# Optimization experiments

Hardware: AMD Instinct MI355X
Metric: run time of the kernel (lower is better)

## Reference

```python
import jax, jax.numpy as jnp
import numpy as np

B, LM, LX, D = 16, 1024, 1024, 768


def setup_inputs() -> dict:
    key = jax.random.key(0)
    k1, k2, k3, k4 = jax.random.split(key, 4)
    main = jax.random.normal(k1, (B, LM, D), dtype=jnp.float32)
    x = jax.random.normal(k2, (B, LX, D), dtype=jnp.float32)
    # keras 'uniform' init ~ U(-0.05, 0.05); scale to keep activations sane
    W = jax.random.uniform(k3, (D, D), dtype=jnp.float32, minval=-0.05, maxval=0.05)
    w = jax.random.uniform(k4, (2 * D, 1), dtype=jnp.float32, minval=-0.05, maxval=0.05)
    return {"main": main, "x": x, "W": W, "w": w}


def reference(main, x, W, w):
    # bilinear co-attention scores: (main @ W) . x^T -> (B, LM, LX)
    proj = jnp.einsum('bmd,de->bme', main, W)            # (B, LM, D)
    scores = jnp.einsum('bme,bne->bmn', proj, x)         # (B, LM, LX) -- no softmax in original
    A = jnp.einsum('bmn,bnd->bmd', scores, x)            # attended features (B, LM, D)
    s = main - A
    m = main * A
    outputs = jnp.concatenate([s, m], axis=-1)           # (B, LM, 2D)
    beta = jnp.einsum('bmk,k->bm', outputs, w[:, 0])     # (B, LM) -- raw, no softmax
    pooled = jnp.einsum('bm,bmk->bk', beta, outputs)     # weighted-sum pooling (B, 2D)
    return pooled
```

## Files before the change

kernel.cpp:

```cpp
#include <hip/hip_runtime.h>

constexpr int kB  = 16;
constexpr int kLM = 1024;
constexpr int kLX = 1024;
constexpr int kD  = 768;

using short8 = __attribute__((ext_vector_type(8))) short;
using f32x4  = __attribute__((ext_vector_type(4))) float;

__device__ __forceinline__ unsigned short f2bf(float f) {
    unsigned u = __float_as_uint(f);
    u = (u + 0x7FFF + ((u >> 16) & 1)) >> 16;
    return (unsigned short)u;
}
__device__ __forceinline__ float bf2f(unsigned short h) {
    return __uint_as_float(((unsigned)h) << 16);
}

__device__ __forceinline__ void gl_lds16(const unsigned short* g, unsigned short* l) {
    auto gp = (const __attribute__((address_space(1))) unsigned int*)g;
    auto lp = (__attribute__((address_space(3))) unsigned int*)l;
    __builtin_amdgcn_global_load_lds(gp, lp, 16, 0, 0);
}

__global__ __launch_bounds__(256) void transpose_cvt_kernel(
    const float* __restrict__ x, unsigned short* __restrict__ xT) {
    __shared__ float tile[64][65];
    const int b  = blockIdx.z;
    const int l0 = blockIdx.x * 64;
    const int d0 = blockIdx.y * 64;
    const int t  = threadIdx.x;
    const int tx = t & 15, ty = t >> 4;
    const float* xb = x + ((size_t)b * kLX + l0) * kD + d0;
#pragma unroll
    for (int p = 0; p < 4; ++p) {
        int r = p * 16 + ty;
        float4 v = *(const float4*)(xb + (size_t)r * kD + tx * 4);
        *(float4*)&tile[r][tx * 4] = v;
    }
    __syncthreads();
    unsigned short* xTb = xT + ((size_t)b * kD + d0) * kLX + l0;
#pragma unroll
    for (int p = 0; p < 4; ++p) {
        int dr = p * 16 + ty;
        ushort4 o;
        o.x = f2bf(tile[tx * 4 + 0][dr]);
        o.y = f2bf(tile[tx * 4 + 1][dr]);
        o.z = f2bf(tile[tx * 4 + 2][dr]);
        o.w = f2bf(tile[tx * 4 + 3][dr]);
        *(ushort4*)(xTb + (size_t)dr * kLX + tx * 4) = o;
    }
}

__global__ __launch_bounds__(256) void cvt_bf16_dual_kernel(
    const float* __restrict__ a, unsigned short* __restrict__ oa, int n4a,
    const float* __restrict__ b, unsigned short* __restrict__ ob, int n4b) {
    int i = blockIdx.x * blockDim.x + threadIdx.x;
    const float* src; unsigned short* dst; int idx;
    if (i < n4a) { src = a; dst = oa; idx = i; }
    else { idx = i - n4a; if (idx >= n4b) return; src = b; dst = ob; }
    float4 v = ((const float4*)src)[idx];
    ushort4 o;
    o.x = f2bf(v.x); o.y = f2bf(v.y); o.z = f2bf(v.z); o.w = f2bf(v.w);
    ((ushort4*)dst)[idx] = o;
}

__global__ __launch_bounds__(256) void gemm_nt_bf16_kernel(
    const unsigned short* __restrict__ A, const unsigned short* __restrict__ B,
    unsigned short* __restrict__ C, int M, int N, int K,
    long sA, long sB, long sC) {
    __shared__ unsigned short Asm[2][128 * 32];
    __shared__ unsigned short Bsm[2][128 * 32];
    const int b  = blockIdx.z;
    const int i0 = blockIdx.x * 128;
    const int j0 = blockIdx.y * 128;
    const int t    = threadIdx.x;
    const int wave = t >> 6, lane = t & 63;
    const int wr = (wave >> 1) * 64, wc = (wave & 1) * 64;
    const int quad = lane >> 4, l15 = lane & 15;

    const unsigned short* Ab = A + (size_t)b * sA + (size_t)i0 * K;
    const unsigned short* Bb = B + (size_t)b * sB + (size_t)j0 * K;

    const int c0 = wave * 64 + lane;
    const int c1 = 256 + wave * 64 + lane;
    auto chunk_off = [&](int c) -> size_t {
        int sr = c >> 3, s = c & 7;
        int tt = s ^ (sr & 7);
        int r  = sr * 2 + (tt >> 2);
        int q  = tt & 3;
        return (size_t)r * K + q * 8;
    };
    const size_t off0 = chunk_off(c0);
    const size_t off1 = chunk_off(c1);

    const int sfr = ((l15 & 1) * 4 + quad) ^ ((l15 >> 1) & 7);
    const int aOff = (wr >> 1) * 64 + (l15 >> 1) * 64 + sfr * 8;
    const int bOff = (wc >> 1) * 64 + (l15 >> 1) * 64 + sfr * 8;

    f32x4 acc[4][4];
    const f32x4 z = {0.f, 0.f, 0.f, 0.f};
#pragma unroll
    for (int i = 0; i < 4; ++i)
#pragma unroll
        for (int j = 0; j < 4; ++j) acc[i][j] = z;

    const int T = K >> 5;
    gl_lds16(Ab + off0, Asm[0] + c0 * 8);
    gl_lds16(Ab + off1, Asm[0] + c1 * 8);
    gl_lds16(Bb + off0, Bsm[0] + c0 * 8);
    gl_lds16(Bb + off1, Bsm[0] + c1 * 8);

    int buf = 0;
    for (int kt = 0; kt < T; ++kt) {
        __syncthreads();
        if (kt + 1 < T) {
            const size_t k = (size_t)(kt + 1) << 5;
            unsigned short* An = Asm[buf ^ 1];
            unsigned short* Bn = Bsm[buf ^ 1];
            gl_lds16(Ab + off0 + k, An + c0 * 8);
            gl_lds16(Ab + off1 + k, An + c1 * 8);
            gl_lds16(Bb + off0 + k, Bn + c0 * 8);
            gl_lds16(Bb + off1 + k, Bn + c1 * 8);
        }
        const unsigned short* aP = Asm[buf] + aOff;
        const unsigned short* bP = Bsm[buf] + bOff;
        short8 af[4], bg[4];
#pragma unroll
        for (int i = 0; i < 4; ++i) af[i] = *(const short8*)(aP + i * 512);
#pragma unroll
        for (int j = 0; j < 4; ++j) bg[j] = *(const short8*)(bP + j * 512);
#pragma unroll
        for (int i = 0; i < 4; ++i)
#pragma unroll
            for (int j = 0; j < 4; ++j)
                acc[i][j] = __builtin_amdgcn_mfma_f32_16x16x32_bf16(
                    af[i], bg[j], acc[i][j], 0, 0, 0);
        buf ^= 1;
    }

    unsigned short* Cb = C + (size_t)b * sC + (size_t)(i0 + wr) * N + j0 + wc;
#pragma unroll
    for (int i = 0; i < 4; ++i)
#pragma unroll
        for (int j = 0; j < 4; ++j)
#pragma unroll
            for (int r = 0; r < 4; ++r)
                Cb[(size_t)(i * 16 + quad * 4 + r) * N + j * 16 + l15] =
                    f2bf(acc[i][j][r]);
}

__global__ __launch_bounds__(256) void pool_kernel(
    const float* __restrict__ mainp, const unsigned short* __restrict__ Aout,
    const float* __restrict__ w, float* __restrict__ out) {
    const int b     = blockIdx.y;
    const int chunk = blockIdx.x;
    const int wave  = threadIdx.x >> 6, lane = threadIdx.x & 63;
    float w1[12], w2[12], ps[12], pm[12];
#pragma unroll
    for (int s = 0; s < 12; ++s) {
        w1[s] = w[s * 64 + lane];
        w2[s] = w[kD + s * 64 + lane];
        ps[s] = 0.f; pm[s] = 0.f;
    }
#pragma unroll
    for (int rr = 0; rr < 4; ++rr) {
        const int row = chunk * 16 + rr * 4 + wave;
        const float* mr = mainp + ((size_t)b * kLM + row) * kD;
        const unsigned short* ar = Aout + ((size_t)b * kLM + row) * kD;
        float sv[12], mv[12], acc = 0.f;
#pragma unroll
        for (int s = 0; s < 12; ++s) {
            float m_ = mr[s * 64 + lane];
            float a_ = bf2f(ar[s * 64 + lane]);
            sv[s] = m_ - a_;
            mv[s] = m_ * a_;
            acc += sv[s] * w1[s] + mv[s] * w2[s];
        }
#pragma unroll
        for (int off = 32; off; off >>= 1) acc += __shfl_xor(acc, off);
#pragma unroll
        for (int s = 0; s < 12; ++s) { ps[s] += acc * sv[s]; pm[s] += acc * mv[s]; }
    }
    float* ob = out + (size_t)b * 2 * kD;
#pragma unroll
    for (int s = 0; s < 12; ++s) {
        atomicAdd(&ob[s * 64 + lane], ps[s]);
        atomicAdd(&ob[kD + s * 64 + lane], pm[s]);
    }
}

extern "C" void kernel_launch(void* const* d_in, const int* in_sizes, int n_in,
                              void* d_out, int out_size, void* d_ws, size_t ws_size,
                              hipStream_t stream) {
    const float* mainp = (const float*)d_in[0];
    const float* x     = (const float*)d_in[1];
    const float* W     = (const float*)d_in[2];
    const float* w     = (const float*)d_in[3];
    float* out = (float*)d_out;

    char* p = (char*)d_ws;
    unsigned short* xT    = (unsigned short*)p; p += (size_t)kB * kD * kLX * 2;
    unsigned short* mainb = (unsigned short*)p; p += (size_t)kB * kLM * kD * 2;
    unsigned short* Wb    = (unsigned short*)p; p += (size_t)kD * kD * 2;
    unsigned short* G     = (unsigned short*)p; p += (size_t)kB * kD * kD * 2;
    unsigned short* Mt    = (unsigned short*)p; p += (size_t)kB * kD * kD * 2;
    unsigned short* Ao    = (unsigned short*)p; p += (size_t)kB * kLM * kD * 2;

    hipMemsetAsync(out, 0, (size_t)kB * 2 * kD * sizeof(float), stream);

    transpose_cvt_kernel<<<dim3(kLX / 64, kD / 64, kB), 256, 0, stream>>>(x, xT);
    {
        int n4a = kB * kLM * kD / 4;
        int n4b = kD * kD / 4;
        cvt_bf16_dual_kernel<<<(n4a + n4b + 255) / 256, 256, 0, stream>>>(
            mainp, mainb, n4a, W, Wb, n4b);
    }
    gemm_nt_bf16_kernel<<<dim3(kD / 128, kD / 128, kB), 256, 0, stream>>>(
        xT, xT, G, kD, kD, kLX, (long)kD * kLX, (long)kD * kLX, (long)kD * kD);
    gemm_nt_bf16_kernel<<<dim3(kD / 128, kD / 128, kB), 256, 0, stream>>>(
        G, Wb, Mt, kD, kD, kD, (long)kD * kD, 0L, (long)kD * kD);
    gemm_nt_bf16_kernel<<<dim3(kLM / 128, kD / 128, kB), 256, 0, stream>>>(
        mainb, Mt, Ao, kLM, kD, kD, (long)kLM * kD, (long)kD * kD, (long)kLM * kD);
    pool_kernel<<<dim3(kLM / 16, kB), 256, 0, stream>>>(mainp, Ao, w, out);
}
```

Measured before the change: 264.8 us.

## Fuse fp32-to-bf16 conversion into GEMM loaders and shrink N tile to 64

Removes the standalone conversion kernel for main and W. The GEMM now loads fp32 operands through registers, converts them to bf16 and writes them into swizzled LDS, with a two-stage register prefetch. The GEMM tile also shrinks from 128x128 to 128x64, with each wave owning 32x64, and launch bounds request 4 blocks per CU. This saves a full pass over main and doubles block count for better CU coverage. In exchange the fp32 loads go through registers instead of direct-to-LDS, main is re-read at fp32 width across N tiles, and per-tile data reuse is lower.

```diff
diff --git a/kernel.cpp b/kernel.cpp
--- a/kernel.cpp
+++ b/kernel.cpp
@@ -21,6 +21,21 @@
     auto gp = (const __attribute__((address_space(1))) unsigned int*)g;
     auto lp = (__attribute__((address_space(3))) unsigned int*)l;
     __builtin_amdgcn_global_load_lds(gp, lp, 16, 0, 0);
+}
+
+__device__ __forceinline__ void writeChunk(unsigned short* dst, float4 lo, float4 hi) {
+    union { short8 v; unsigned short u[8]; } o;
+    o.u[0] = f2bf(lo.x); o.u[1] = f2bf(lo.y); o.u[2] = f2bf(lo.z); o.u[3] = f2bf(lo.w);
+    o.u[4] = f2bf(hi.x); o.u[5] = f2bf(hi.y); o.u[6] = f2bf(hi.z); o.u[7] = f2bf(hi.w);
+    *(short8*)dst = o.v;
+}
+
+__device__ __forceinline__ size_t chunk_off(int c, int K) {
+    int sr = c >> 3, s = c & 7;
+    int tt = s ^ (sr & 7);
+    int r  = sr * 2 + (tt >> 2);
+    int q  = tt & 3;
+    return (size_t)r * K + q * 8;
 }
 
 __global__ __launch_bounds__(256) void transpose_cvt_kernel(
@@ -52,86 +67,117 @@
     }
 }
 
-__global__ __launch_bounds__(256) void cvt_bf16_dual_kernel(
-    const float* __restrict__ a, unsigned short* __restrict__ oa, int n4a,
-    const float* __restrict__ b, unsigned short* __restrict__ ob, int n4b) {
-    int i = blockIdx.x * blockDim.x + threadIdx.x;
-    const float* src; unsigned short* dst; int idx;
-    if (i < n4a) { src = a; dst = oa; idx = i; }
-    else { idx = i - n4a; if (idx >= n4b) return; src = b; dst = ob; }
-    float4 v = ((const float4*)src)[idx];
-    ushort4 o;
-    o.x = f2bf(v.x); o.y = f2bf(v.y); o.z = f2bf(v.z); o.w = f2bf(v.w);
-    ((ushort4*)dst)[idx] = o;
-}
-
-__global__ __launch_bounds__(256) void gemm_nt_bf16_kernel(
-    const unsigned short* __restrict__ A, const unsigned short* __restrict__ B,
+template <bool AFP32, bool BFP32>
+__global__ __launch_bounds__(256, 4) void gemm_nt_kernel(
+    const void* __restrict__ Av, const void* __restrict__ Bv,
     unsigned short* __restrict__ C, int M, int N, int K,
     long sA, long sB, long sC) {
     __shared__ unsigned short Asm[2][128 * 32];
-    __shared__ unsigned short Bsm[2][128 * 32];
+    __shared__ unsigned short Bsm[2][64 * 32];
     const int b  = blockIdx.z;
     const int i0 = blockIdx.x * 128;
-    const int j0 = blockIdx.y * 128;
+    const int j0 = blockIdx.y * 64;
     const int t    = threadIdx.x;
     const int wave = t >> 6, lane = t & 63;
-    const int wr = (wave >> 1) * 64, wc = (wave & 1) * 64;
     const int quad = lane >> 4, l15 = lane & 15;
 
-    const unsigned short* Ab = A + (size_t)b * sA + (size_t)i0 * K;
-    const unsigned short* Bb = B + (size_t)b * sB + (size_t)j0 * K;
-
-    const int c0 = wave * 64 + lane;
-    const int c1 = 256 + wave * 64 + lane;
-    auto chunk_off = [&](int c) -> size_t {
-        int sr = c >> 3, s = c & 7;
-        int tt = s ^ (sr & 7);
-        int r  = sr * 2 + (tt >> 2);
-        int q  = tt & 3;
-        return (size_t)r * K + q * 8;
-    };
-    const size_t off0 = chunk_off(c0);
-    const size_t off1 = chunk_off(c1);
-
-    const int sfr = ((l15 & 1) * 4 + quad) ^ ((l15 >> 1) & 7);
-    const int aOff = (wr >> 1) * 64 + (l15 >> 1) * 64 + sfr * 8;
-    const int bOff = (wc >> 1) * 64 + (l15 >> 1) * 64 + sfr * 8;
-
-    f32x4 acc[4][4];
+    const unsigned short* Abh = AFP32 ? nullptr
+        : (const unsigned short*)Av + (size_t)b * sA + (size_t)i0 * K;
+    const unsigned short* Bbh = BFP32 ? nullptr
+        : (const unsigned short*)Bv + (size_t)b * sB + (size_t)j0 * K;
+    const float* Abf = AFP32
+        ? (const float*)Av + (size_t)b * sA + (size_t)i0 * K : nullptr;
+    const float* Bbf = BFP32
+        ? (const float*)Bv + (size_t)b * sB + (size_t)j0 * K : nullptr;
+
+    const int cA0 = t, cA1 = t + 256, cB = t;
+    const size_t offA0 = chunk_off(cA0, K);
+    const size_t offA1 = chunk_off(cA1, K);
+    const size_t offB  = chunk_off(cB, K);
+
+    const int sfr  = ((l15 & 1) * 4 + quad) ^ ((l15 >> 1) & 7);
+    const int aOff = wave * 1024 + (l15 >> 1) * 64 + sfr * 8;
+    const int bOff = (l15 >> 1) * 64 + sfr * 8;
+
+    f32x4 acc[2][4];
     const f32x4 z = {0.f, 0.f, 0.f, 0.f};
 #pragma unroll
-    for (int i = 0; i < 4; ++i)
+    for (int i = 0; i < 2; ++i)
 #pragma unroll
         for (int j = 0; j < 4; ++j) acc[i][j] = z;
 
     const int T = K >> 5;
-    gl_lds16(Ab + off0, Asm[0] + c0 * 8);
-    gl_lds16(Ab + off1, Asm[0] + c1 * 8);
-    gl_lds16(Bb + off0, Bsm[0] + c0 * 8);
-    gl_lds16(Bb + off1, Bsm[0] + c1 * 8);
+    float4 pa0, pa1, pa2, pa3, pb0, pb1;
+
+    if constexpr (AFP32) {
+        float4 a0 = *(const float4*)(Abf + offA0);
+        float4 a1 = *(const float4*)(Abf + offA0 + 4);
+        float4 a2 = *(const float4*)(Abf + offA1);
+        float4 a3 = *(const float4*)(Abf + offA1 + 4);
+        writeChunk(Asm[0] + cA0 * 8, a0, a1);
+        writeChunk(Asm[0] + cA1 * 8, a2, a3);
+    } else {
+        gl_lds16(Abh + offA0, Asm[0] + cA0 * 8);
+        gl_lds16(Abh + offA1, Asm[0] + cA1 * 8);
+    }
+    if constexpr (BFP32) {
+        float4 b0 = *(const float4*)(Bbf + offB);
+        float4 b1 = *(const float4*)(Bbf + offB + 4);
+        writeChunk(Bsm[0] + cB * 8, b0, b1);
+    } else {
+        gl_lds16(Bbh + offB, Bsm[0] + cB * 8);
+    }
+    if constexpr (AFP32) {
+        pa0 = *(const float4*)(Abf + offA0 + 32);
+        pa1 = *(const float4*)(Abf + offA0 + 36);
+        pa2 = *(const float4*)(Abf + offA1 + 32);
+        pa3 = *(const float4*)(Abf + offA1 + 36);
+    }
+    if constexpr (BFP32) {
+        pb0 = *(const float4*)(Bbf + offB + 32);
+        pb1 = *(const float4*)(Bbf + offB + 36);
+    }
 
     int buf = 0;
     for (int kt = 0; kt < T; ++kt) {
         __syncthreads();
         if (kt + 1 < T) {
             const size_t k = (size_t)(kt + 1) << 5;
-            unsigned short* An = Asm[buf ^ 1];
-            unsigned short* Bn = Bsm[buf ^ 1];
-            gl_lds16(Ab + off0 + k, An + c0 * 8);
-            gl_lds16(Ab + off1 + k, An + c1 * 8);
-            gl_lds16(Bb + off0 + k, Bn + c0 * 8);
-            gl_lds16(Bb + off1 + k, Bn + c1 * 8);
+            if constexpr (AFP32) {
+                writeChunk(Asm[buf ^ 1] + cA0 * 8, pa0, pa1);
+                writeChunk(Asm[buf ^ 1] + cA1 * 8, pa2, pa3);
+            } else {
+                gl_lds16(Abh + offA0 + k, Asm[buf ^ 1] + cA0 * 8);
+                gl_lds16(Abh + offA1 + k, Asm[buf ^ 1] + cA1 * 8);
+            }
+            if constexpr (BFP32) {
+                writeChunk(Bsm[buf ^ 1] + cB * 8, pb0, pb1);
+            } else {
+                gl_lds16(Bbh + offB + k, Bsm[buf ^ 1] + cB * 8);
+            }
+        }
+        if (kt + 2 < T) {
+            const size_t k2 = (size_t)(kt + 2) << 5;
+            if constexpr (AFP32) {
+                pa0 = *(const float4*)(Abf + offA0 + k2);
+                pa1 = *(const float4*)(Abf + offA0 + k2 + 4);
+                pa2 = *(const float4*)(Abf + offA1 + k2);
+                pa3 = *(const float4*)(Abf + offA1 + k2 + 4);
+            }
+            if constexpr (BFP32) {
+                pb0 = *(const float4*)(Bbf + offB + k2);
+                pb1 = *(const float4*)(Bbf + offB + k2 + 4);
+            }
         }
         const unsigned short* aP = Asm[buf] + aOff;
         const unsigned short* bP = Bsm[buf] + bOff;
-        short8 af[4], bg[4];
-#pragma unroll
-        for (int i = 0; i < 4; ++i) af[i] = *(const short8*)(aP + i * 512);
+        short8 af[2], bg[4];
+#pragma unroll
+        for (int i = 0; i < 2; ++i) af[i] = *(const short8*)(aP + i * 512);
 #pragma unroll
         for (int j = 0; j < 4; ++j) bg[j] = *(const short8*)(bP + j * 512);
 #pragma unroll
-        for (int i = 0; i < 4; ++i)
+        for (int i = 0; i < 2; ++i)
 #pragma unroll
             for (int j = 0; j < 4; ++j)
                 acc[i][j] = __builtin_amdgcn_mfma_f32_16x16x32_bf16(
@@ -139,9 +185,9 @@
         buf ^= 1;
     }
 
-    unsigned short* Cb = C + (size_t)b * sC + (size_t)(i0 + wr) * N + j0 + wc;
-#pragma unroll
-    for (int i = 0; i < 4; ++i)
+    unsigned short* Cb = C + (size_t)b * sC + (size_t)(i0 + wave * 32) * N + j0;
+#pragma unroll
+    for (int i = 0; i < 2; ++i)
 #pragma unroll
         for (int j = 0; j < 4; ++j)
 #pragma unroll
@@ -200,27 +246,21 @@
     float* out = (float*)d_out;
 
     char* p = (char*)d_ws;
-    unsigned short* xT    = (unsigned short*)p; p += (size_t)kB * kD * kLX * 2;
-    unsigned short* mainb = (unsigned short*)p; p += (size_t)kB * kLM * kD * 2;
-    unsigned short* Wb    = (unsigned short*)p; p += (size_t)kD * kD * 2;
-    unsigned short* G     = (unsigned short*)p; p += (size_t)kB * kD * kD * 2;
-    unsigned short* Mt    = (unsigned short*)p; p += (size_t)kB * kD * kD * 2;
-    unsigned short* Ao    = (unsigned short*)p; p += (size_t)kB * kLM * kD * 2;
+    unsigned short* xT = (unsigned short*)p; p += (size_t)kB * kD * kLX * 2;
+    unsigned short* G  = (unsigned short*)p; p += (size_t)kB * kD * kD * 2;
+    unsigned short* Mt = (unsigned short*)p; p += (size_t)kB * kD * kD * 2;
+    unsigned short* Ao = (unsigned short*)p; p += (size_t)kB * kLM * kD * 2;
 
     hipMemsetAsync(out, 0, (size_t)kB * 2 * kD * sizeof(float), stream);
 
     transpose_cvt_kernel<<<dim3(kLX / 64, kD / 64, kB), 256, 0, stream>>>(x, xT);
-    {
-        int n4a = kB * kLM * kD / 4;
-        int n4b = kD * kD / 4;
-        cvt_bf16_dual_kernel<<<(n4a + n4b + 255) / 256, 256, 0, stream>>>(
-            mainp, mainb, n4a, W, Wb, n4b);
-    }
-    gemm_nt_bf16_kernel<<<dim3(kD / 128, kD / 128, kB), 256, 0, stream>>>(
+
+    gemm_nt_kernel<false, false><<<dim3(kD / 128, kD / 64, kB), 256, 0, stream>>>(
         xT, xT, G, kD, kD, kLX, (long)kD * kLX, (long)kD * kLX, (long)kD * kD);
-    gemm_nt_bf16_kernel<<<dim3(kD / 128, kD / 128, kB), 256, 0, stream>>>(
-        G, Wb, Mt, kD, kD, kD, (long)kD * kD, 0L, (long)kD * kD);
-    gemm_nt_bf16_kernel<<<dim3(kLM / 128, kD / 128, kB), 256, 0, stream>>>(
-        mainb, Mt, Ao, kLM, kD, kD, (long)kLM * kD, (long)kD * kD, (long)kLM * kD);
+    gemm_nt_kernel<false, true><<<dim3(kD / 128, kD / 64, kB), 256, 0, stream>>>(
+        G, W, Mt, kD, kD, kD, (long)kD * kD, 0L, (long)kD * kD);
+    gemm_nt_kernel<true, false><<<dim3(kLM / 128, kD / 64, kB), 256, 0, stream>>>(
+        mainp, Mt, Ao, kLM, kD, kD, (long)kLM * kD, (long)kD * kD, (long)kLM * kD);
+
     pool_kernel<<<dim3(kLM / 16, kB), 256, 0, stream>>>(mainp, Ao, w, out);
 }
```

Result: slower. 294.0 us (+11.1%).
